# Kernel tuning notes

Hardware: AMD Instinct MI355X
Metric: run time of the kernel (lower is better)

The kernel has to match this reference:

```python
import jax, jax.numpy as jnp
import numpy as np

B, S, N = 64, 256, 512


def setup_inputs() -> dict:
    key = jax.random.key(0)
    ks = jax.random.split(key, 8)
    x = jax.random.normal(ks[0], (B, S, N), dtype=jnp.float32)
    # sparse adjacency, no self loops (module assumes adj has no self-loop)
    adj = (jax.random.uniform(ks[1], (N, N)) < 0.05).astype(jnp.float32)
    adj = adj * (1.0 - jnp.eye(N, dtype=jnp.float32))
    W = jax.random.uniform(ks[2], (N, N), dtype=jnp.float32)  # torch.rand init
    parent_node_weigh = jax.random.uniform(ks[3], (N,), dtype=jnp.float32)
    bound = 1.0 / np.sqrt(N)  # torch Linear default init
    Wq_w = jax.random.uniform(ks[4], (N, N), minval=-bound, maxval=bound, dtype=jnp.float32)
    Wq_b = jax.random.uniform(ks[5], (N,), minval=-bound, maxval=bound, dtype=jnp.float32)
    Wk_w = jax.random.uniform(ks[6], (N, N), minval=-bound, maxval=bound, dtype=jnp.float32)
    Wk_b = jax.random.uniform(ks[7], (N,), minval=-bound, maxval=bound, dtype=jnp.float32)
    return {"x": x, "adj": adj, "W": W, "parent_node_weigh": parent_node_weigh,
            "Wq_w": Wq_w, "Wq_b": Wq_b, "Wk_w": Wk_w, "Wk_b": Wk_b}


def reference(x, adj, W, parent_node_weigh, Wq_w, Wq_b, Wk_w, Wk_b):
    # x: (B,S,N). Q,K = Linear(x).permute(0,2,1) -> (B,N,S)
    Q = jnp.einsum('bsk,nk->bns', x, Wq_w) + Wq_b[None, :, None]
    K = jnp.einsum('bsk,nk->bns', x, Wk_w) + Wk_b[None, :, None]
    xt = jnp.transpose(x, (0, 2, 1))  # (B,N,S)
    n = adj.shape[0]
    # Algebraic equivalent of the repeat/mask/matmul/bmm chain:
    # Att[b,m,n] = adj[m,n] * sum_j W[m,j] * adj[j,n] * <K[b,j,:], Q[b,n,:]>
    S_kq = jnp.einsum('bjs,bns->bjn', K, Q)  # (B,N,N)
    Att = adj * jnp.einsum('mj,bjn->bmn', W, adj[:, :, None].transpose(2, 0, 1)[0][None] * S_kq if False else adj[None, :, :] * S_kq)
    Att = Att + jnp.diag(parent_node_weigh)[None, :, :]
    cycle_adj = jnp.eye(n, dtype=adj.dtype) + adj
    Att = jax.nn.softmax(Att, axis=1) * cycle_adj  # softmax over dim=1 (torch dim=1)
    agg_x = jnp.einsum('bmn,bms->bns', Att, xt)  # Att^T @ x
    return (agg_x, Att)
```

## Files before the change

### kernel.cpp

```cpp
#include <hip/hip_runtime.h>
#include <hip/hip_fp16.h>
#include <cstdint>
#include <cmath>

#define BB 64
#define SS 256
#define NN 512
#define MAXC 64
#define MAXC1 (MAXC + 1)

typedef float f32x4 __attribute__((ext_vector_type(4)));
typedef _Float16 half8 __attribute__((ext_vector_type(8)));

__device__ __forceinline__ unsigned short f2h(float f) {
  return __half_as_ushort(__float2half(f));
}
__device__ __forceinline__ float h2f(unsigned short u) {
  return __half2float(__ushort_as_half(u));
}
__device__ __forceinline__ float2 unpackh2(uint32_t u) {
  return make_float2(__half2float(__ushort_as_half((unsigned short)(u & 0xffffu))),
                     __half2float(__ushort_as_half((unsigned short)(u >> 16))));
}

__device__ __forceinline__ void gload_lds16(const void* g, void* s) {
  __builtin_amdgcn_global_load_lds(
      (const __attribute__((address_space(1))) uint32_t*)g,
      (__attribute__((address_space(3))) uint32_t*)s, 16, 0, 0);
}

__global__ __launch_bounds__(256) void k_prep0(const float* __restrict__ adj,
                                               int* __restrict__ col_idx,
                                               int* __restrict__ col_cnt,
                                               const float* __restrict__ Wq,
                                               const float* __restrict__ Wk,
                                               unsigned short* __restrict__ Wqp,
                                               unsigned short* __restrict__ Wkp) {
  if (blockIdx.x < 128) {
    const int n = blockIdx.x * 4 + (threadIdx.x >> 6);
    const int lane = threadIdx.x & 63;
    int cnt = 0;
    for (int m0 = 0; m0 < NN; m0 += 64) {
      const int m = m0 + lane;
      const float a = adj[(size_t)m * NN + n];
      unsigned long long mask = __ballot(a != 0.0f);
      const int prefix = __popcll(mask & ((1ull << lane) - 1ull));
      if (a != 0.0f && cnt + prefix < MAXC) col_idx[n * MAXC + cnt + prefix] = m;
      cnt += __popcll(mask);
    }
    if (lane == 0) col_cnt[n] = (cnt > MAXC) ? MAXC : cnt;
  } else {
    const int n = blockIdx.x - 128;
    const int half = threadIdx.x >> 7;
    const float* src = half ? Wk : Wq;
    unsigned short* dst = half ? Wkp : Wqp;
    const int k = (threadIdx.x & 127) * 4;
    float4 v = *(const float4*)(src + (size_t)n * NN + k);
    ushort4 o;
    o.x = f2h(v.x); o.y = f2h(v.y); o.z = f2h(v.z); o.w = f2h(v.w);
    *(ushort4*)(dst + (size_t)n * 512 + k) = o;
  }
}

__global__ __launch_bounds__(256) void k_wsub(const float* __restrict__ W,
                                              const int* __restrict__ col_idx,
                                              const int* __restrict__ col_cnt,
                                              int* __restrict__ col_off,
                                              float* __restrict__ Wsub) {
  const int n = blockIdx.x;
  const int t = threadIdx.x;
  const int wave = t >> 6, lane = t & 63;
  __shared__ int lsh[MAXC];
  __shared__ int preSh;
  const int c = col_cnt[n];
  if (wave == 0) {
    int pre = 0;
#pragma unroll
    for (int i0 = 0; i0 < NN; i0 += 64) {
      const int i = i0 + lane;
      const int cc = col_cnt[i];
      pre += (i < n) ? cc * cc : 0;
    }
#pragma unroll
    for (int off = 32; off; off >>= 1) pre += __shfl_xor(pre, off);
    if (lane == 0) { col_off[n] = pre; preSh = pre; }
    if (lane < c) lsh[lane] = col_idx[n * MAXC + lane];
  }
  __syncthreads();
  if (lane < c) {
    const float* Wm = W + (size_t)lsh[lane] * NN;
    float* dst = Wsub + preSh + lane;
    for (int ji = wave; ji < c; ji += 4)
      dst[(size_t)ji * c] = Wm[lsh[ji]];
  }
}

__global__ __launch_bounds__(256) void k_xprep(const float* __restrict__ x,
                                               unsigned short* __restrict__ xp,
                                               unsigned short* __restrict__ xt,
                                               float* __restrict__ Att) {
  __shared__ float tile[32][33];
  const int b = blockIdx.z;
  const int s0 = blockIdx.x * 32, n0 = blockIdx.y * 32;
  const float* xb = x + (size_t)b * SS * NN;
  const int tx = threadIdx.x, ty = threadIdx.y;
#pragma unroll
  for (int i = ty; i < 32; i += 8) {
    const float v = xb[(size_t)(s0 + i) * NN + n0 + tx];
    tile[i][tx] = v;
    xp[(size_t)(b * SS + s0 + i) * 512 + n0 + tx] = f2h(v);
  }
  {
    const int bid = (blockIdx.z * 16 + blockIdx.y) * 8 + blockIdx.x;
    const int t = ty * 32 + tx;
    f32x4* dst = (f32x4*)(Att + (size_t)bid * 2048);
    const f32x4 z = (f32x4)0.0f;
    dst[t] = z;
    dst[t + 256] = z;
  }
  __syncthreads();
  unsigned short* xtb = xt + (size_t)b * NN * SS;
#pragma unroll
  for (int i = ty; i < 32; i += 8)
    xtb[(size_t)(n0 + i) * SS + s0 + tx] = f2h(tile[tx][i]);
}

__global__ __launch_bounds__(256, 2) void k_lin2(const unsigned short* __restrict__ Wqp,
                                                 const unsigned short* __restrict__ Wkp,
                                                 const float* __restrict__ bq,
                                                 const float* __restrict__ bk,
                                                 const unsigned short* __restrict__ xp,
                                                 unsigned short* __restrict__ Qt,
                                                 unsigned short* __restrict__ Kt) {
  __shared__ __align__(16) char sm[49152];
  const int t = threadIdx.x;
  const int w = t >> 6, l = t & 63;
  const int id = blockIdx.x;
  const int xcd = id & 7, sub = id >> 3;
  const int bn0 = (xcd * 16 + (sub >> 2)) * 128;
  const int bm0 = (sub & 3) * 128;

  const int swz = (((l & 3) ^ ((l >> 3) & 3))) * 16;
  const char* srcb[6];
  char* dstb[6];
#pragma unroll
  for (int i = 0; i < 6; i++) {
    const int ch = w * 6 + i;
    const int panel = ch >> 3, rowgrp = ch & 7;
    const int row = rowgrp * 16 + (l >> 2);
    const char* g0 = (panel == 0) ? (const char*)Wqp
                   : (panel == 1) ? (const char*)Wkp : (const char*)xp;
    const int gr = ((panel == 2) ? bn0 : bm0) + row;
    srcb[i] = g0 + (size_t)gr * 1024 + swz;
    dstb[i] = sm + panel * 8192 + rowgrp * 1024 + l * 16;
  }

  const int fr = l & 15, fg = l >> 4;
  const int mrow = (w >> 1) * 64, ncol = (w & 1) * 64;
  const int slot = (fg ^ ((fr >> 1) & 3)) * 16;
  int offQ[4], offK[4], offB[4];
#pragma unroll
  for (int fm = 0; fm < 4; fm++) {
    offQ[fm] = (mrow + fm * 16 + fr) * 64 + slot;
    offK[fm] = 8192 + (mrow + fm * 16 + fr) * 64 + slot;
    offB[fm] = 16384 + (ncol + fm * 16 + fr) * 64 + slot;
  }

  f32x4 accq[4][4], acck[4][4];
#pragma unroll
  for (int i = 0; i < 4; i++)
#pragma unroll
    for (int j = 0; j < 4; j++) { accq[i][j] = (f32x4)0.0f; acck[i][j] = (f32x4)0.0f; }

#pragma unroll
  for (int i = 0; i < 6; i++) gload_lds16(srcb[i], dstb[i]);
  __syncthreads();

  int cur = 0;
  for (int kk = 0; kk < 16; kk++) {
    if (kk + 1 < 16) {
      const int ko = (kk + 1) * 64;
      const int boff = (cur ^ 1) * 24576;
#pragma unroll
      for (int i = 0; i < 6; i++)
        gload_lds16(srcb[i] + ko, dstb[i] + boff);
    }
    const char* base = sm + cur * 24576;
    half8 afq[4], afk[4];
#pragma unroll
    for (int fm = 0; fm < 4; fm++) {
      afq[fm] = *(const half8*)(base + offQ[fm]);
      afk[fm] = *(const half8*)(base + offK[fm]);
    }
#pragma unroll
    for (int fn = 0; fn < 4; fn++) {
      const half8 bv = *(const half8*)(base + offB[fn]);
#pragma unroll
      for (int fm = 0; fm < 4; fm++) {
        accq[fm][fn] = __builtin_amdgcn_mfma_f32_16x16x32_f16(afq[fm], bv, accq[fm][fn], 0, 0, 0);
        acck[fm][fn] = __builtin_amdgcn_mfma_f32_16x16x32_f16(afk[fm], bv, acck[fm][fn], 0, 0, 0);
      }
    }
    __syncthreads();
    cur ^= 1;
  }

  const int b = bn0 >> 8;
  const int sbase = (bn0 & 255) + ncol;
#pragma unroll
  for (int fm = 0; fm < 4; fm++) {
#pragma unroll
    for (int q = 0; q < 4; q++) {
      const int n = bm0 + mrow + fm * 16 + fg * 4 + q;
      const float bvq = bq[n];
      const float bvk = bk[n];
#pragma unroll
      for (int fn = 0; fn < 4; fn++) {
        const int s = sbase + fn * 16 + fr;
        Qt[((size_t)b * NN + n) * SS + s] = f2h(accq[fm][fn][q] + bvq);
        Kt[((size_t)b * NN + n) * SS + s] = f2h(acck[fm][fn][q] + bvk);
      }
    }
  }
}

__global__ __launch_bounds__(256, 2) void k_gram(const unsigned short* __restrict__ Qt,
                                                 const unsigned short* __restrict__ Kt,
                                                 unsigned short* __restrict__ ST) {
  __shared__ __align__(16) char sm[32768];
  const int t = threadIdx.x;
  const int w = t >> 6, l = t & 63;
  const int id = blockIdx.x;
  const int xcd = id & 7, rest = id >> 3;
  const int batch = (xcd << 3) + (rest >> 4);
  const int tile = rest & 15;
  const int m0 = (tile >> 2) * 128;
  const int n0 = (tile & 3) * 128;

  const int swz = (((l & 3) ^ ((l >> 3) & 3))) * 16;
  const char* srcb[4];
  char* dstb[4];
#pragma unroll
  for (int i = 0; i < 4; i++) {
    const int ch = w * 4 + i;
    const int panel = ch >> 3, rowgrp = ch & 7;
    const int row = rowgrp * 16 + (l >> 2);
    const char* g0 = panel ? (const char*)Kt : (const char*)Qt;
    const int gr = (panel ? n0 : m0) + row;
    srcb[i] = g0 + ((size_t)batch * 512 + gr) * 512 + swz;
    dstb[i] = sm + panel * 8192 + rowgrp * 1024 + l * 16;
  }

  const int fr = l & 15, fg = l >> 4;
  const int mrow = (w >> 1) * 64, ncol = (w & 1) * 64;
  const int slot = (fg ^ ((fr >> 1) & 3)) * 16;
  int offA[4], offB[4];
#pragma unroll
  for (int fm = 0; fm < 4; fm++) {
    offA[fm] = (mrow + fm * 16 + fr) * 64 + slot;
    offB[fm] = 8192 + (ncol + fm * 16 + fr) * 64 + slot;
  }

  f32x4 acc[4][4];
#pragma unroll
  for (int i = 0; i < 4; i++)
#pragma unroll
    for (int j = 0; j < 4; j++) acc[i][j] = (f32x4)0.0f;

#pragma unroll
  for (int i = 0; i < 4; i++) gload_lds16(srcb[i], dstb[i]);
  __syncthreads();

  int cur = 0;
  for (int kk = 0; kk < 8; kk++) {
    if (kk + 1 < 8) {
      const int ko = (kk + 1) * 64;
      const int boff = (cur ^ 1) * 16384;
#pragma unroll
      for (int i = 0; i < 4; i++)
        gload_lds16(srcb[i] + ko, dstb[i] + boff);
    }
    const char* base = sm + cur * 16384;
    half8 af[4];
#pragma unroll
    for (int fm = 0; fm < 4; fm++)
      af[fm] = *(const half8*)(base + offA[fm]);
#pragma unroll
    for (int fn = 0; fn < 4; fn++) {
      const half8 bv = *(const half8*)(base + offB[fn]);
#pragma unroll
      for (int fm = 0; fm < 4; fm++)
        acc[fm][fn] = __builtin_amdgcn_mfma_f32_16x16x32_f16(af[fm], bv, acc[fm][fn], 0, 0, 0);
    }
    __syncthreads();
    cur ^= 1;
  }

  unsigned short* STb = ST + (size_t)batch * NN * NN;
#pragma unroll
  for (int fm = 0; fm < 4; fm++) {
#pragma unroll
    for (int q = 0; q < 4; q++) {
      const int n = m0 + mrow + fm * 16 + fg * 4 + q;
#pragma unroll
      for (int fn = 0; fn < 4; fn++) {
        const int j = n0 + ncol + fn * 16 + fr;
        STb[(size_t)n * NN + j] = f2h(acc[fm][fn][q]);
      }
    }
  }
}

__global__ __launch_bounds__(256) void k_fused(const unsigned short* __restrict__ ST,
                                               const unsigned short* __restrict__ xt,
                                               const float* __restrict__ Wsub,
                                               const float* __restrict__ pnw,
                                               const int* __restrict__ col_idx,
                                               const int* __restrict__ col_cnt,
                                               const int* __restrict__ col_off,
                                               float* __restrict__ Att,
                                               float* __restrict__ agg) {
  const int id = blockIdx.x;
  const int xcd = id & 7;
  const int r = id >> 3;
  const int n = r & 511;
  const int bgrp = r >> 9;
  const int t = threadIdx.x;
  const int wave = t >> 6, lane = t & 63;
  const int b = (xcd << 3) + (bgrp << 2) + wave;

  __shared__ int   lsh[MAXC + 1];
  __shared__ int   lshB[MAXC + 1];
  __shared__ float Wsh[MAXC * MAXC];
  __shared__ float vsh[4][MAXC];
  __shared__ float ash[4][MAXC + 1];

  const int c = col_cnt[n];

  unsigned short stv = 0;
  if (lane < c) {
    const int myIdx = col_idx[n * MAXC + lane];
    stv = ST[((size_t)b * NN + n) * NN + myIdx];
  }

  if (t < c) {
    const int v = col_idx[n * MAXC + t];
    lsh[t] = v;
    lshB[t] = v << 9;
  }
  if (t == c) { lsh[c] = n; lshB[c] = n << 9; }
  {
    const int cc = c * c;
    const float* Wp = Wsub + col_off[n];
    for (int i = t; i < cc; i += 256) Wsh[i] = Wp[i];
  }
  __syncthreads();

  if (lane < c) vsh[wave][lane] = h2f(stv);

  float aval = 0.0f;
  if (lane < c) {
    for (int ji = 0; ji < c; ji++)
      aval += Wsh[ji * c + lane] * vsh[wave][ji];
  }

  const float dlg = pnw[n];
  float mval = (lane < c) ? aval : -INFINITY;
#pragma unroll
  for (int off = 32; off; off >>= 1) mval = fmaxf(mval, __shfl_xor(mval, off));
  const float colmax = fmaxf(mval, fmaxf(dlg, 0.0f));
  const float e = (lane < c) ? __expf(aval - colmax) : 0.0f;
  float sum = e;
#pragma unroll
  for (int off = 32; off; off >>= 1) sum += __shfl_xor(sum, off);
  const float denom = sum + __expf(dlg - colmax)
                    + (float)(NN - c - 1) * __expf(-colmax);
  const float inv = 1.0f / denom;

  float* Acol = Att + (size_t)b * NN * NN + n;
  if (lane < c) {
    const float attv = e * inv;
    ash[wave][lane] = attv;
    Acol[(size_t)lsh[lane] * NN] = attv;
  }
  if (lane == c) {
    const float dv = __expf(dlg - colmax) * inv;
    ash[wave][c] = dv;
    Acol[(size_t)n * NN] = dv;
  }

  const char* xtb = (const char*)(xt + (size_t)b * NN * SS);
  f32x4 acc = (f32x4)0.0f;
  for (int mi = 0; mi <= c; mi++) {
    const float a = ash[wave][mi];
    const uint2 v = *(const uint2*)(xtb + lshB[mi] + lane * 8);
    const float2 x01 = unpackh2(v.x);
    const float2 x23 = unpackh2(v.y);
    acc.x += a * x01.x;
    acc.y += a * x01.y;
    acc.z += a * x23.x;
    acc.w += a * x23.y;
  }
  *(f32x4*)(agg + ((size_t)b * NN + n) * SS + lane * 4) = acc;
}

extern "C" void kernel_launch(void* const* d_in, const int* in_sizes, int n_in,
                              void* d_out, int out_size, void* d_ws, size_t ws_size,
                              hipStream_t stream) {
  const float* x    = (const float*)d_in[0];
  const float* adj  = (const float*)d_in[1];
  const float* W    = (const float*)d_in[2];
  const float* pnw  = (const float*)d_in[3];
  const float* Wq_w = (const float*)d_in[4];
  const float* Wq_b = (const float*)d_in[5];
  const float* Wk_w = (const float*)d_in[6];
  const float* Wk_b = (const float*)d_in[7];

  float* agg = (float*)d_out;
  float* Att = (float*)d_out + (size_t)BB * NN * SS;

  char* p = (char*)d_ws;
  unsigned short* xp  = (unsigned short*)p; p += (size_t)BB * SS * 512 * 2;
  unsigned short* Wqp = (unsigned short*)p; p += (size_t)NN * 512 * 2;
  unsigned short* Wkp = (unsigned short*)p; p += (size_t)NN * 512 * 2;
  unsigned short* Qt  = (unsigned short*)p; p += (size_t)BB * NN * SS * 2;
  unsigned short* Kt  = (unsigned short*)p; p += (size_t)BB * NN * SS * 2;
  unsigned short* xt  = (unsigned short*)p; p += (size_t)BB * NN * SS * 2;
  unsigned short* ST  = (unsigned short*)p; p += (size_t)BB * NN * NN * 2;
  float* Wsub = (float*)p; p += (size_t)NN * MAXC * MAXC * 4;
  int* col_idx = (int*)p; p += (size_t)NN * MAXC * 4;
  int* col_cnt = (int*)p; p += NN * 4;
  int* col_off = (int*)p;

  k_prep0<<<dim3(640), dim3(256), 0, stream>>>(adj, col_idx, col_cnt,
                                               Wq_w, Wk_w, Wqp, Wkp);
  k_wsub<<<dim3(NN), dim3(256), 0, stream>>>(W, col_idx, col_cnt, col_off, Wsub);
  k_xprep<<<dim3(SS / 32, NN / 32, BB), dim3(32, 8), 0, stream>>>(x, xp, xt, Att);

  k_lin2<<<dim3(512), dim3(256), 0, stream>>>(Wqp, Wkp, Wq_b, Wk_b, xp, Qt, Kt);
  k_gram<<<dim3(1024), dim3(256), 0, stream>>>(Qt, Kt, ST);
  k_fused<<<dim3(8192), dim3(256), 0, stream>>>(ST, xt, Wsub, pnw,
                                                col_idx, col_cnt, col_off,
                                                Att, agg);
}
```

Measured before the change: 116.2 us.

## Replace sparse gather aggregation with dense fp16 MFMA GEMM over attention matrix

The sparse per-column gather over the transposed x copy is replaced. k_fused now writes a dense fp16 row of each attention column (mostly zeros) into a new workspace buffer, and a new k_agg kernel computes agg as a dense MFMA GEMM of that buffer against xp. This removes the transposed xt buffer and the tiled transpose in k_xprep, which becomes a flat vectorised fp16 conversion plus zero-fill. In exchange it writes and reads a full 64x512x512 fp16 attention buffer and does dense GEMM work, although only about 5% of the entries are nonzero.

```diff
diff --git a/kernel.cpp b/kernel.cpp
--- a/kernel.cpp
+++ b/kernel.cpp
@@ -7,7 +7,6 @@
 #define SS 256
 #define NN 512
 #define MAXC 64
-#define MAXC1 (MAXC + 1)
 
 typedef float f32x4 __attribute__((ext_vector_type(4)));
 typedef _Float16 half8 __attribute__((ext_vector_type(8)));
@@ -17,10 +16,6 @@
 }
 __device__ __forceinline__ float h2f(unsigned short u) {
   return __half2float(__ushort_as_half(u));
-}
-__device__ __forceinline__ float2 unpackh2(uint32_t u) {
-  return make_float2(__half2float(__ushort_as_half((unsigned short)(u & 0xffffu))),
-                     __half2float(__ushort_as_half((unsigned short)(u >> 16))));
 }
 
 __device__ __forceinline__ void gload_lds16(const void* g, void* s) {
@@ -97,32 +92,17 @@
 
 __global__ __launch_bounds__(256) void k_xprep(const float* __restrict__ x,
                                                unsigned short* __restrict__ xp,
-                                               unsigned short* __restrict__ xt,
                                                float* __restrict__ Att) {
-  __shared__ float tile[32][33];
-  const int b = blockIdx.z;
-  const int s0 = blockIdx.x * 32, n0 = blockIdx.y * 32;
-  const float* xb = x + (size_t)b * SS * NN;
-  const int tx = threadIdx.x, ty = threadIdx.y;
-#pragma unroll
-  for (int i = ty; i < 32; i += 8) {
-    const float v = xb[(size_t)(s0 + i) * NN + n0 + tx];
-    tile[i][tx] = v;
-    xp[(size_t)(b * SS + s0 + i) * 512 + n0 + tx] = f2h(v);
-  }
-  {
-    const int bid = (blockIdx.z * 16 + blockIdx.y) * 8 + blockIdx.x;
-    const int t = ty * 32 + tx;
-    f32x4* dst = (f32x4*)(Att + (size_t)bid * 2048);
-    const f32x4 z = (f32x4)0.0f;
-    dst[t] = z;
-    dst[t + 256] = z;
-  }
-  __syncthreads();
-  unsigned short* xtb = xt + (size_t)b * NN * SS;
-#pragma unroll
-  for (int i = ty; i < 32; i += 8)
-    xtb[(size_t)(n0 + i) * SS + s0 + tx] = f2h(tile[tx][i]);
+  const int t = threadIdx.x;
+  const size_t base = ((size_t)blockIdx.x * 256 + t) * 4;
+  float4 v = *(const float4*)(x + base);
+  ushort4 o;
+  o.x = f2h(v.x); o.y = f2h(v.y); o.z = f2h(v.z); o.w = f2h(v.w);
+  *(ushort4*)(xp + base) = o;
+  f32x4* dst = (f32x4*)(Att + (size_t)blockIdx.x * 2048);
+  const f32x4 z = (f32x4)0.0f;
+  dst[t] = z;
+  dst[t + 256] = z;
 }
 
 __global__ __launch_bounds__(256, 2) void k_lin2(const unsigned short* __restrict__ Wqp,
@@ -312,14 +292,13 @@
 }
 
 __global__ __launch_bounds__(256) void k_fused(const unsigned short* __restrict__ ST,
-                                               const unsigned short* __restrict__ xt,
                                                const float* __restrict__ Wsub,
                                                const float* __restrict__ pnw,
                                                const int* __restrict__ col_idx,
                                                const int* __restrict__ col_cnt,
                                                const int* __restrict__ col_off,
                                                float* __restrict__ Att,
-                                               float* __restrict__ agg) {
+                                               unsigned short* __restrict__ Att2) {
   const int id = blockIdx.x;
   const int xcd = id & 7;
   const int r = id >> 3;
@@ -330,10 +309,9 @@
   const int b = (xcd << 3) + (bgrp << 2) + wave;
 
   __shared__ int   lsh[MAXC + 1];
-  __shared__ int   lshB[MAXC + 1];
   __shared__ float Wsh[MAXC * MAXC];
   __shared__ float vsh[4][MAXC];
-  __shared__ float ash[4][MAXC + 1];
+  __shared__ unsigned short ush[4][NN];
 
   const int c = col_cnt[n];
 
@@ -343,12 +321,11 @@
     stv = ST[((size_t)b * NN + n) * NN + myIdx];
   }
 
-  if (t < c) {
-    const int v = col_idx[n * MAXC + t];
-    lsh[t] = v;
-    lshB[t] = v << 9;
-  }
-  if (t == c) { lsh[c] = n; lshB[c] = n << 9; }
+#pragma unroll
+  for (int j = 0; j < 8; j++) ush[wave][lane * 8 + j] = 0;
+
+  if (t < c) lsh[t] = col_idx[n * MAXC + t];
+  if (t == c) lsh[c] = n;
   {
     const int cc = c * c;
     const float* Wp = Wsub + col_off[n];
@@ -380,28 +357,112 @@
   float* Acol = Att + (size_t)b * NN * NN + n;
   if (lane < c) {
     const float attv = e * inv;
-    ash[wave][lane] = attv;
     Acol[(size_t)lsh[lane] * NN] = attv;
+    ush[wave][lsh[lane]] = f2h(attv);
   }
   if (lane == c) {
     const float dv = __expf(dlg - colmax) * inv;
-    ash[wave][c] = dv;
     Acol[(size_t)n * NN] = dv;
-  }
-
-  const char* xtb = (const char*)(xt + (size_t)b * NN * SS);
-  f32x4 acc = (f32x4)0.0f;
-  for (int mi = 0; mi <= c; mi++) {
-    const float a = ash[wave][mi];
-    const uint2 v = *(const uint2*)(xtb + lshB[mi] + lane * 8);
-    const float2 x01 = unpackh2(v.x);
-    const float2 x23 = unpackh2(v.y);
-    acc.x += a * x01.x;
-    acc.y += a * x01.y;
-    acc.z += a * x23.x;
-    acc.w += a * x23.y;
-  }
-  *(f32x4*)(agg + ((size_t)b * NN + n) * SS + lane * 4) = acc;
+    ush[wave][n] = f2h(dv);
+  }
+
+  uint32_t pk[4];
+#pragma unroll
+  for (int j = 0; j < 4; j++) {
+    const uint32_t lo = ush[wave][lane * 8 + j * 2];
+    const uint32_t hi = ush[wave][lane * 8 + j * 2 + 1];
+    pk[j] = lo | (hi << 16);
+  }
+  uint4 o = make_uint4(pk[0], pk[1], pk[2], pk[3]);
+  *(uint4*)((char*)Att2 + ((size_t)b * NN + n) * 1024 + lane * 16) = o;
+}
+
+__global__ __launch_bounds__(256, 2) void k_agg(const unsigned short* __restrict__ Att2,
+                                                const unsigned short* __restrict__ xp,
+                                                float* __restrict__ agg) {
+  __shared__ __align__(16) char sm[32768];
+  const int t = threadIdx.x;
+  const int w = t >> 6, l = t & 63;
+  const int id = blockIdx.x;
+  const int xcd = id & 7, rest = id >> 3;
+  const int batch = (xcd << 3) + (rest >> 3);
+  const int tile = rest & 7;
+  const int m0 = (tile >> 1) * 128;
+  const int s0 = (tile & 1) * 128;
+
+  const int swz = (((l & 3) ^ ((l >> 3) & 3))) * 16;
+  const char* srcb[4];
+  char* dstb[4];
+#pragma unroll
+  for (int i = 0; i < 4; i++) {
+    const int ch = w * 4 + i;
+    const int panel = ch >> 3, rowgrp = ch & 7;
+    const int row = rowgrp * 16 + (l >> 2);
+    const char* g0 = panel ? (const char*)xp : (const char*)Att2;
+    const size_t gr = panel ? ((size_t)batch * SS + s0 + row)
+                            : ((size_t)batch * NN + m0 + row);
+    srcb[i] = g0 + gr * 1024 + swz;
+    dstb[i] = sm + panel * 8192 + rowgrp * 1024 + l * 16;
+  }
+
+  const int fr = l & 15, fg = l >> 4;
+  const int mrow = (w >> 1) * 64, ncol = (w & 1) * 64;
+  const int slot = (fg ^ ((fr >> 1) & 3)) * 16;
+  int offA[4], offB[4];
+#pragma unroll
+  for (int fm = 0; fm < 4; fm++) {
+    offA[fm] = (mrow + fm * 16 + fr) * 64 + slot;
+    offB[fm] = 8192 + (ncol + fm * 16 + fr) * 64 + slot;
+  }
+
+  f32x4 acc[4][4];
+#pragma unroll
+  for (int i = 0; i < 4; i++)
+#pragma unroll
+    for (int j = 0; j < 4; j++) acc[i][j] = (f32x4)0.0f;
+
+#pragma unroll
+  for (int i = 0; i < 4; i++) gload_lds16(srcb[i], dstb[i]);
+  __syncthreads();
+
+  int cur = 0;
+  for (int kk = 0; kk < 16; kk++) {
+    if (kk + 1 < 16) {
+      const int ko = (kk + 1) * 64;
+      const int boff = (cur ^ 1) * 16384;
+#pragma unroll
+      for (int i = 0; i < 4; i++)
+        gload_lds16(srcb[i] + ko, dstb[i] + boff);
+    }
+    const char* base = sm + cur * 16384;
+    half8 af[4];
+#pragma unroll
+    for (int fm = 0; fm < 4; fm++)
+      af[fm] = *(const half8*)(base + offA[fm]);
+#pragma unroll
+    for (int fn = 0; fn < 4; fn++) {
+      const half8 bv = *(const half8*)(base + offB[fn]);
+#pragma unroll
+      for (int fm = 0; fm < 4; fm++)
+        acc[fm][fn] = __builtin_amdgcn_mfma_f32_16x16x32_f16(af[fm], bv, acc[fm][fn], 0, 0, 0);
+    }
+    __syncthreads();
+    cur ^= 1;
+  }
+
+  float* ab = agg + (size_t)batch * NN * SS;
+#pragma unroll
+  for (int fm = 0; fm < 4; fm++) {
+#pragma unroll
+    for (int q = 0; q < 4; q++) {
+      const int n = m0 + mrow + fm * 16 + fg * 4 + q;
+#pragma unroll
+      for (int fn = 0; fn < 4; fn++) {
+        const int s = s0 + ncol + fn * 16 + fr;
+        ab[(size_t)n * SS + s] = acc[fm][fn][q];
+      }
+    }
+  }
 }
 
 extern "C" void kernel_launch(void* const* d_in, const int* in_sizes, int n_in,
@@ -425,8 +486,8 @@
   unsigned short* Wkp = (unsigned short*)p; p += (size_t)NN * 512 * 2;
   unsigned short* Qt  = (unsigned short*)p; p += (size_t)BB * NN * SS * 2;
   unsigned short* Kt  = (unsigned short*)p; p += (size_t)BB * NN * SS * 2;
-  unsigned short* xt  = (unsigned short*)p; p += (size_t)BB * NN * SS * 2;
   unsigned short* ST  = (unsigned short*)p; p += (size_t)BB * NN * NN * 2;
+  unsigned short* At2 = (unsigned short*)p; p += (size_t)BB * NN * NN * 2;
   float* Wsub = (float*)p; p += (size_t)NN * MAXC * MAXC * 4;
   int* col_idx = (int*)p; p += (size_t)NN * MAXC * 4;
   int* col_cnt = (int*)p; p += NN * 4;
@@ -435,11 +496,12 @@
   k_prep0<<<dim3(640), dim3(256), 0, stream>>>(adj, col_idx, col_cnt,
                                                Wq_w, Wk_w, Wqp, Wkp);
   k_wsub<<<dim3(NN), dim3(256), 0, stream>>>(W, col_idx, col_cnt, col_off, Wsub);
-  k_xprep<<<dim3(SS / 32, NN / 32, BB), dim3(32, 8), 0, stream>>>(x, xp, xt, Att);
+  k_xprep<<<dim3(8192), dim3(256), 0, stream>>>(x, xp, Att);
 
   k_lin2<<<dim3(512), dim3(256), 0, stream>>>(Wqp, Wkp, Wq_b, Wk_b, xp, Qt, Kt);
   k_gram<<<dim3(1024), dim3(256), 0, stream>>>(Qt, Kt, ST);
-  k_fused<<<dim3(8192), dim3(256), 0, stream>>>(ST, xt, Wsub, pnw,
+  k_fused<<<dim3(8192), dim3(256), 0, stream>>>(ST, Wsub, pnw,
                                                 col_idx, col_cnt, col_off,
-                                                Att, agg);
-}
+                                                Att, At2);
+  k_agg<<<dim3(512), dim3(256), 0, stream>>>(At2, xp, agg);
+}
```

Result: faster. 111.3 us (-4.3%).
